# Kernel optimization log

Measured on AMD Instinct MI355X. Metric: run time of the kernel, lower is better.

The kernel has to match this reference:

```python
import jax, jax.numpy as jnp
import numpy as np
import math

N, T, D = 1024, 4096, 20


def setup_inputs() -> dict:
    key = jax.random.key(0)
    k1, k2, k3, k4, k5 = jax.random.split(key, 5)
    evidence_vector = jax.random.normal(k1, (T, D), jnp.float32)
    # valid (strictly positive) prior and row-stochastic, all-positive transitions
    prior_probs = jax.nn.softmax(jax.random.normal(k2, (N,), jnp.float32))
    transition_probs = jax.nn.softmax(jax.random.normal(k3, (N, N), jnp.float32), axis=1)
    means = jax.random.normal(k4, (N, D), jnp.float32)
    stds = jax.random.uniform(k5, (N, D), jnp.float32, minval=0.5, maxval=1.5)
    emission_paras = jnp.stack([means, stds], axis=-1)  # [N, D, 2]
    return {"evidence_vector": evidence_vector, "prior_probs": prior_probs,
            "transition_probs": transition_probs, "emission_paras": emission_paras}


def _emission_logp(evidence, emission_paras):
    # Faithful to the source: p = (2*pi*std)**(-0.5) * exp(-(x-mean)^2/(2*std^2))
    mean = emission_paras[..., 0]  # [N, D]
    std = emission_paras[..., 1]   # [N, D]
    p = (2.0 * math.pi * std) ** (-0.5) * jnp.exp(
        -(evidence[:, None, :] - mean) ** 2 / (2.0 * std ** 2))  # [T, N, D]
    logp = jnp.log(p)
    # step 0 uses raw log; steps >=1 pass through nan_to_num(nan=0, inf kept)
    logp0 = jnp.sum(logp[0], axis=1)  # [N]
    logp_rest = jnp.sum(jnp.nan_to_num(logp[1:], nan=0.0, posinf=jnp.inf, neginf=-jnp.inf), axis=2)  # [T-1, N]
    return logp0, logp_rest


def _viterbi_nl(evidence, prior, trans, emission_paras):
    logp0, logp_rest = _emission_logp(evidence, emission_paras)
    log_trans = jnp.log(trans)  # all positive transitions -> finite
    col0 = jnp.log(prior) + logp0  # [N]

    state_ids = jnp.arange(N)

    def step(prev_col, logp_t):
        # scores[k, j] = nl[k, i-1] + log trans[k, j]; nl[j,i] = max_k scores + logp
        scores = prev_col[:, None] + log_trans          # [N, N]
        best = jnp.max(scores, axis=0)                  # [N]
        # j == 0 branch of the source: prev_state = j, no max over k
        new0 = prev_col[0] + log_trans[0, 0]
        new_col = jnp.where(state_ids == 0, new0, best) + logp_t
        return new_col, new_col

    _, cols = jax.lax.scan(step, col0, logp_rest)       # [T-1, N]
    nl = jnp.concatenate([col0[None, :], cols], axis=0).T  # [N, T]
    return nl, log_trans


def reference(evidence_vector, prior_probs, transition_probs, emission_paras):
    nl, log_trans = _viterbi_nl(evidence_vector, prior_probs, transition_probs, emission_paras)
    last = jnp.argmax(nl[:, -1]).astype(jnp.int32)

    def bt_step(front, i):
        # argmax_j nl[j, i] + log trans[j, front]; strict '>' ascending -> first max
        best = jnp.argmax(nl[:, i] + log_trans[:, front]).astype(jnp.int32)
        return best, best

    _, rev = jax.lax.scan(bt_step, last, jnp.arange(T - 2, -1, -1))
    # source appends the final argmax twice, then prepends states for i = T-2..0
    sequence = jnp.concatenate([rev[::-1], jnp.array([last, last], dtype=jnp.int32)])
    return sequence  # [T + 1] int32
```

## Files before the change

### kernel.cpp

```cpp
#include <hip/hip_runtime.h>
#include <math.h>

#define NSTATES 1024
#define TT      4096
#define DD      20

#define FW_BLOCKS  64
#define FW_THREADS 256
#define JPB  16
#define NSEG 16
#define KSEG 64

#define SENT 0x7FC00000u

#define OFF_COLS  ((size_t)20 << 20)
#define OFF_PTR   ((size_t)36 << 20)

typedef unsigned int u32;

#define ALD(p) __hip_atomic_load((p), __ATOMIC_RELAXED, __HIP_MEMORY_SCOPE_AGENT)

__global__ __launch_bounds__(FW_THREADS, 1) void k_forward(
    const float* __restrict__ tr, const float* __restrict__ ev,
    const float* __restrict__ epar, const float* __restrict__ prior,
    float* __restrict__ cols, unsigned short* __restrict__ bptr,
    u32* __restrict__ ready)
{
    __shared__ __align__(16) float prevs[NSEG * 68];
    __shared__ float          smaxw[4][JPB];
    __shared__ unsigned short sidxw[4][JPB];
    __shared__ float          elp[2][JPB][DD];
    const int tid  = threadIdx.x;
    const int seg  = tid >> 4;
    const int jj   = tid & (JPB - 1);
    const int wav  = tid >> 6;
    const int j0   = blockIdx.x * JPB;
    const int j    = j0 + jj;

    {
        uint4* mine = (uint4*)cols + (size_t)blockIdx.x * (NSTATES * TT / 4 / FW_BLOCKS);
        const uint4 sv = make_uint4(SENT, SENT, SENT, SENT);
        #pragma unroll
        for (int i = 0; i < (NSTATES * TT / 4 / FW_BLOCKS) / FW_THREADS; ++i)
            mine[i * FW_THREADS + tid] = sv;
    }

    const float lat00 = logf(tr[0]);
    float4 latr[16];
    #pragma unroll
    for (int u = 0; u < 16; ++u) {
        #pragma unroll
        for (int i = 0; i < 4; ++i) {
            int k = seg * KSEG + u * 4 + i;
            ((float*)&latr[u])[i] = logf(tr[(size_t)k * NSTATES + j]);
        }
    }

    const int jj0e = tid / DD, d0e = tid % DD;
    const float m0 = epar[((size_t)(j0 + jj0e) * DD + d0e) * 2 + 0];
    const float s0 = epar[((size_t)(j0 + jj0e) * DD + d0e) * 2 + 1];
    const float coef0 = 1.0f / sqrtf(6.2831853071795864769f * s0);
    const float den0  = 2.0f * (s0 * s0);
    const bool  has1  = (tid + 256) < JPB * DD;
    const int   it1   = tid + 256;
    const int jj1e = has1 ? it1 / DD : 0, d1e = has1 ? it1 % DD : 0;
    const float m1 = has1 ? epar[((size_t)(j0 + jj1e) * DD + d1e) * 2 + 0] : 0.0f;
    const float s1 = has1 ? epar[((size_t)(j0 + jj1e) * DD + d1e) * 2 + 1] : 1.0f;
    const float coef1 = 1.0f / sqrtf(6.2831853071795864769f * s1);
    const float den1  = 2.0f * (s1 * s1);

    auto emis = [&](int t, int buf) {
        float x0  = ev[(size_t)t * DD + d0e];
        float df0 = x0 - m0;
        float num0 = df0 * df0;
        float p0  = coef0 * expf(-num0 / den0);
        elp[buf][jj0e][d0e] = logf(p0);
        if (has1) {
            float x1  = ev[(size_t)t * DD + d1e];
            float df1 = x1 - m1;
            float num1 = df1 * df1;
            float p1  = coef1 * expf(-num1 / den1);
            elp[buf][jj1e][d1e] = logf(p1);
        }
    };

    __syncthreads();
    if (tid == 0) {
        asm volatile("s_waitcnt vmcnt(0)" ::: "memory");
        __hip_atomic_fetch_add(ready, 1u, __ATOMIC_RELEASE,
                               __HIP_MEMORY_SCOPE_AGENT);
        while (ALD(ready) < (u32)FW_BLOCKS) __builtin_amdgcn_s_sleep(2);
    }
    __syncthreads();

    float* dstp = &prevs[(tid >> 4) * 68 + (tid & 15) * 4];
    const float* rowp = &prevs[seg * 68];

    emis(0, 0);
    __syncthreads();
    if (tid < JPB) {
        float acc = 0.0f;
        #pragma unroll
        for (int d = 0; d < DD; ++d) acc += elp[0][tid][d];
        float c0 = logf(prior[j0 + tid]) + acc;
        __hip_atomic_store((u32*)cols + (j0 + tid), __float_as_uint(c0),
                           __ATOMIC_RELAXED, __HIP_MEMORY_SCOPE_AGENT);
    }
    __syncthreads();
    emis(1, 1);
    __syncthreads();
    float esum_reg = 0.0f;
    if (tid < JPB) {
        #pragma unroll
        for (int d = 0; d < DD; ++d) esum_reg += elp[1][tid][d];
    }

    for (int t = 1; t < TT; ++t) {
        const u32* p = (const u32*)(cols + (size_t)(t - 1) * NSTATES) + tid * 4;
        u32 w0, w1, w2, w3;
        for (;;) {
            w0 = __hip_atomic_load(p + 0, __ATOMIC_RELAXED, __HIP_MEMORY_SCOPE_AGENT);
            w1 = __hip_atomic_load(p + 1, __ATOMIC_RELAXED, __HIP_MEMORY_SCOPE_AGENT);
            w2 = __hip_atomic_load(p + 2, __ATOMIC_RELAXED, __HIP_MEMORY_SCOPE_AGENT);
            w3 = __hip_atomic_load(p + 3, __ATOMIC_RELAXED, __HIP_MEMORY_SCOPE_AGENT);
            if (w0 != SENT && w1 != SENT && w2 != SENT && w3 != SENT) break;
            __builtin_amdgcn_s_sleep(1);
        }
        {
            float4 v;
            v.x = __uint_as_float(w0);
            v.y = __uint_as_float(w1);
            v.z = __uint_as_float(w2);
            v.w = __uint_as_float(w3);
            *(float4*)dstp = v;
        }
        __syncthreads();

        float best = -__builtin_inff();
        int bidx = seg * KSEG;
        #pragma unroll
        for (int u = 0; u < 16; ++u) {
            float4 q  = *(const float4*)(rowp + u * 4);
            float4 wv = latr[u];
            int k0 = seg * KSEG + u * 4;
            float v0 = q.x + wv.x;
            float v1 = q.y + wv.y;
            float v2 = q.z + wv.z;
            float v3 = q.w + wv.w;
            if (v0 > best) { best = v0; bidx = k0;     }
            if (v1 > best) { best = v1; bidx = k0 + 1; }
            if (v2 > best) { best = v2; bidx = k0 + 2; }
            if (v3 > best) { best = v3; bidx = k0 + 3; }
        }

        {
            float ov = __shfl_xor(best, 16);
            int   oi = __shfl_xor(bidx, 16);
            if (ov > best || (ov == best && oi < bidx)) { best = ov; bidx = oi; }
            ov = __shfl_xor(best, 32);
            oi = __shfl_xor(bidx, 32);
            if (ov > best || (ov == best && oi < bidx)) { best = ov; bidx = oi; }
        }
        if ((tid & 63) < JPB) {
            smaxw[wav][jj] = best;
            sidxw[wav][jj] = (unsigned short)bidx;
        }
        __syncthreads();

        if (tid < JPB) {
            float m = smaxw[0][tid];
            int  mi = sidxw[0][tid];
            #pragma unroll
            for (int ww = 1; ww < 4; ++ww) {
                float v = smaxw[ww][tid];
                if (v > m) { m = v; mi = sidxw[ww][tid]; }
            }
            int jw = j0 + tid;
            float val = (jw == 0) ? (prevs[0] + lat00) : m;
            float out = val + esum_reg;
            __hip_atomic_store((u32*)(cols + (size_t)t * NSTATES) + jw,
                               __float_as_uint(out), __ATOMIC_RELAXED,
                               __HIP_MEMORY_SCOPE_AGENT);
            bptr[(size_t)t * NSTATES + jw] = (unsigned short)mi;
        }

        if (t + 1 < TT) {
            emis(t + 1, (t + 1) & 1);
            __syncthreads();
            if (tid < JPB) {
                float acc = 0.0f;
                #pragma unroll
                for (int d = 0; d < DD; ++d) acc += elp[(t + 1) & 1][tid][d];
                esum_reg = acc;
            }
        }
    }
}

#define BTC 24
__global__ void k_backtrace(const float* __restrict__ lastcol,
                            const unsigned short* __restrict__ bptr,
                            int* __restrict__ seq)
{
    __shared__ unsigned short ring[2][BTC][NSTATES];
    __shared__ int s_front;
    const int tid = threadIdx.x;

    if (tid < 64) {
        float best = -__builtin_inff();
        int bi = 0;
        for (int n2 = tid; n2 < NSTATES; n2 += 64) {
            float v = lastcol[n2];
            if (v > best) { best = v; bi = n2; }
        }
        #pragma unroll
        for (int off = 32; off > 0; off >>= 1) {
            float ov = __shfl_xor(best, off);
            int   oi = __shfl_xor(bi, off);
            if (ov > best || (ov == best && oi < bi)) { best = ov; bi = oi; }
        }
        if (tid == 0) { seq[TT] = bi; seq[TT - 1] = bi; s_front = bi; }
    }
    __syncthreads();

    auto stage = [&](int c, int buf, int t0, int stride) {
        int rhi = TT - 1 - c * BTC;
        int rlo = rhi - (BTC - 1); if (rlo < 1) rlo = 1;
        int n4 = (rhi - rlo + 1) * 128;
        uint4* dst = (uint4*)&ring[buf][0][0];
        for (int idx = t0; idx < n4; idx += stride) {
            int ro = idx >> 7, wo = idx & 127;
            dst[idx] = ((const uint4*)(bptr + (size_t)(rhi - ro) * NSTATES))[wo];
        }
    };
    const int nc = (TT - 1 + BTC - 1) / BTC;
    stage(0, 0, tid, 256);
    __syncthreads();
    for (int c = 0; c < nc; ++c) {
        int buf = c & 1;
        if (tid != 0) {
            if (c + 1 < nc) stage(c + 1, buf ^ 1, tid - 1, 255);
        } else {
            int rhi = TT - 1 - c * BTC;
            int rlo = rhi - (BTC - 1); if (rlo < 1) rlo = 1;
            int front = s_front;
            for (int r = rhi; r >= rlo; --r) {
                front = (int)ring[buf][rhi - r][front];
                seq[r - 1] = front;
            }
            s_front = front;
        }
        __syncthreads();
    }
}

extern "C" void kernel_launch(void* const* d_in, const int* in_sizes, int n_in,
                              void* d_out, int out_size, void* d_ws, size_t ws_size,
                              hipStream_t stream) {
    const float* ev    = (const float*)d_in[0];
    const float* prior = (const float*)d_in[1];
    const float* tr    = (const float*)d_in[2];
    const float* epar  = (const float*)d_in[3];
    int* seq = (int*)d_out;
    char* ws = (char*)d_ws;
    float* cols = (float*)(ws + OFF_COLS);
    unsigned short* bptr = (unsigned short*)(ws + OFF_PTR);
    u32* ready = (u32*)(ws + OFF_PTR);

    hipMemsetAsync(ready, 0, 4, stream);
    k_forward<<<FW_BLOCKS, FW_THREADS, 0, stream>>>(tr, ev, epar, prior,
                                                    cols, bptr, ready);
    k_backtrace<<<1, 256, 0, stream>>>(cols + (size_t)(TT - 1) * NSTATES, bptr, seq);
}
```

Baseline: 9.452 ms.

## Parallelize Viterbi backtrace across 64 blocks via composed segment maps

The backtrace moves from one sequential block to 64 blocks, each owning 64 rows of backpointers in LDS. Each block composes its rows into a full state-to-state map, block 0 chains these maps to find each segment's entry state, and then every block walks its own segment in parallel. This replaces a single serial walk through 4095 dependent rows with parallel map composition, a short 64-step chain and 64-row walks. In exchange it adds an inter-block spin-wait that relies on all 64 blocks being resident at once, and the forward kernel's ready counter moves to the start of the workspace.

Result: faster. 8.678 ms (-8.2%).

```diff
diff --git a/kernel.cpp b/kernel.cpp
--- a/kernel.cpp
+++ b/kernel.cpp
@@ -19,6 +19,7 @@
 typedef unsigned int u32;
 
 #define ALD(p) __hip_atomic_load((p), __ATOMIC_RELAXED, __HIP_MEMORY_SCOPE_AGENT)
+#define AST(p, v) __hip_atomic_store((p), (v), __ATOMIC_RELAXED, __HIP_MEMORY_SCOPE_AGENT)
 
 __global__ __launch_bounds__(FW_THREADS, 1) void k_forward(
     const float* __restrict__ tr, const float* __restrict__ ev,
@@ -103,8 +104,7 @@
         #pragma unroll
         for (int d = 0; d < DD; ++d) acc += elp[0][tid][d];
         float c0 = logf(prior[j0 + tid]) + acc;
-        __hip_atomic_store((u32*)cols + (j0 + tid), __float_as_uint(c0),
-                           __ATOMIC_RELAXED, __HIP_MEMORY_SCOPE_AGENT);
+        AST((u32*)cols + (j0 + tid), __float_as_uint(c0));
     }
     __syncthreads();
     emis(1, 1);
@@ -119,10 +119,10 @@
         const u32* p = (const u32*)(cols + (size_t)(t - 1) * NSTATES) + tid * 4;
         u32 w0, w1, w2, w3;
         for (;;) {
-            w0 = __hip_atomic_load(p + 0, __ATOMIC_RELAXED, __HIP_MEMORY_SCOPE_AGENT);
-            w1 = __hip_atomic_load(p + 1, __ATOMIC_RELAXED, __HIP_MEMORY_SCOPE_AGENT);
-            w2 = __hip_atomic_load(p + 2, __ATOMIC_RELAXED, __HIP_MEMORY_SCOPE_AGENT);
-            w3 = __hip_atomic_load(p + 3, __ATOMIC_RELAXED, __HIP_MEMORY_SCOPE_AGENT);
+            w0 = ALD(p + 0);
+            w1 = ALD(p + 1);
+            w2 = ALD(p + 2);
+            w3 = ALD(p + 3);
             if (w0 != SENT && w1 != SENT && w2 != SENT && w3 != SENT) break;
             __builtin_amdgcn_s_sleep(1);
         }
@@ -178,9 +178,7 @@
             int jw = j0 + tid;
             float val = (jw == 0) ? (prevs[0] + lat00) : m;
             float out = val + esum_reg;
-            __hip_atomic_store((u32*)(cols + (size_t)t * NSTATES) + jw,
-                               __float_as_uint(out), __ATOMIC_RELAXED,
-                               __HIP_MEMORY_SCOPE_AGENT);
+            AST((u32*)(cols + (size_t)t * NSTATES) + jw, __float_as_uint(out));
             bptr[(size_t)t * NSTATES + jw] = (unsigned short)mi;
         }
 
@@ -197,60 +195,79 @@
     }
 }
 
-#define BTC 24
-__global__ void k_backtrace(const float* __restrict__ lastcol,
-                            const unsigned short* __restrict__ bptr,
-                            int* __restrict__ seq)
+#define SEGR 64
+__global__ __launch_bounds__(256, 1) void k_backtrace(
+    const float* __restrict__ lastcol, const unsigned short* __restrict__ bptr,
+    int* __restrict__ seq, u32* __restrict__ ctrl,
+    u32* __restrict__ entries, u32* __restrict__ maps)
 {
-    __shared__ unsigned short ring[2][BTC][NSTATES];
-    __shared__ int s_front;
+    __shared__ unsigned short rows[SEGR][NSTATES];
+    __shared__ int s_last;
     const int tid = threadIdx.x;
-
-    if (tid < 64) {
-        float best = -__builtin_inff();
-        int bi = 0;
-        for (int n2 = tid; n2 < NSTATES; n2 += 64) {
-            float v = lastcol[n2];
-            if (v > best) { best = v; bi = n2; }
-        }
-        #pragma unroll
-        for (int off = 32; off > 0; off >>= 1) {
-            float ov = __shfl_xor(best, off);
-            int   oi = __shfl_xor(bi, off);
-            if (ov > best || (ov == best && oi < bi)) { best = ov; bi = oi; }
-        }
-        if (tid == 0) { seq[TT] = bi; seq[TT - 1] = bi; s_front = bi; }
-    }
-    __syncthreads();
-
-    auto stage = [&](int c, int buf, int t0, int stride) {
-        int rhi = TT - 1 - c * BTC;
-        int rlo = rhi - (BTC - 1); if (rlo < 1) rlo = 1;
-        int n4 = (rhi - rlo + 1) * 128;
-        uint4* dst = (uint4*)&ring[buf][0][0];
-        for (int idx = t0; idx < n4; idx += stride) {
-            int ro = idx >> 7, wo = idx & 127;
-            dst[idx] = ((const uint4*)(bptr + (size_t)(rhi - ro) * NSTATES))[wo];
-        }
-    };
-    const int nc = (TT - 1 + BTC - 1) / BTC;
-    stage(0, 0, tid, 256);
-    __syncthreads();
-    for (int c = 0; c < nc; ++c) {
-        int buf = c & 1;
-        if (tid != 0) {
-            if (c + 1 < nc) stage(c + 1, buf ^ 1, tid - 1, 255);
-        } else {
-            int rhi = TT - 1 - c * BTC;
-            int rlo = rhi - (BTC - 1); if (rlo < 1) rlo = 1;
-            int front = s_front;
-            for (int r = rhi; r >= rlo; --r) {
-                front = (int)ring[buf][rhi - r][front];
-                seq[r - 1] = front;
-            }
-            s_front = front;
+    const int s   = blockIdx.x;
+    const int lo  = (s == 0) ? 1 : s * SEGR;
+    const int hi  = s * SEGR + SEGR - 1;
+    const int nrows = hi - lo + 1;
+
+    for (int idx = tid; idx < nrows * 128; idx += 256) {
+        int ro = idx >> 7, wo = idx & 127;
+        ((uint4*)&rows[ro][0])[wo] =
+            ((const uint4*)(bptr + (size_t)(lo + ro) * NSTATES))[wo];
+    }
+    __syncthreads();
+
+    int f0 = tid * 4, f1 = tid * 4 + 1, f2 = tid * 4 + 2, f3 = tid * 4 + 3;
+    for (int r = hi; r >= lo; --r) {
+        const unsigned short* row = &rows[r - lo][0];
+        f0 = row[f0]; f1 = row[f1]; f2 = row[f2]; f3 = row[f3];
+    }
+    AST(maps + (size_t)s * 512 + 2 * tid,     (u32)f0 | ((u32)f1 << 16));
+    AST(maps + (size_t)s * 512 + 2 * tid + 1, (u32)f2 | ((u32)f3 << 16));
+    __syncthreads();
+    if (tid == 0)
+        __hip_atomic_fetch_add(ctrl + 1, 1u, __ATOMIC_RELEASE,
+                               __HIP_MEMORY_SCOPE_AGENT);
+
+    if (s == 0) {
+        if (tid < 64) {
+            float best = -__builtin_inff();
+            int bi = 0;
+            for (int n2 = tid; n2 < NSTATES; n2 += 64) {
+                float v = lastcol[n2];
+                if (v > best) { best = v; bi = n2; }
+            }
+            #pragma unroll
+            for (int off = 32; off > 0; off >>= 1) {
+                float ov = __shfl_xor(best, off);
+                int   oi = __shfl_xor(bi, off);
+                if (ov > best || (ov == best && oi < bi)) { best = ov; bi = oi; }
+            }
+            if (tid == 0) s_last = bi;
         }
         __syncthreads();
+        if (tid == 0) {
+            while (ALD(ctrl + 1) < 64u) __builtin_amdgcn_s_sleep(2);
+            int last = s_last;
+            seq[TT] = last; seq[TT - 1] = last;
+            u32 entry = (u32)last;
+            for (int ss = 63; ss >= 1; --ss) {
+                AST(entries + ss, entry);
+                u32 w = ALD(maps + (size_t)ss * 512 + (entry >> 1));
+                entry = (entry & 1) ? (w >> 16) : (w & 0xFFFFu);
+            }
+            AST(entries + 0, entry);
+            asm volatile("s_waitcnt vmcnt(0)" ::: "memory");
+            AST(ctrl + 2, 1u);
+        }
+    }
+
+    if (tid == 0) {
+        while (ALD(ctrl + 2) == 0u) __builtin_amdgcn_s_sleep(2);
+        u32 front = ALD(entries + s);
+        for (int r = hi; r >= lo; --r) {
+            front = rows[r - lo][front];
+            seq[r - 1] = (int)front;
+        }
     }
 }
 
@@ -265,10 +282,13 @@
     char* ws = (char*)d_ws;
     float* cols = (float*)(ws + OFF_COLS);
     unsigned short* bptr = (unsigned short*)(ws + OFF_PTR);
-    u32* ready = (u32*)(ws + OFF_PTR);
-
-    hipMemsetAsync(ready, 0, 4, stream);
+    u32* ctrl    = (u32*)ws;
+    u32* entries = (u32*)(ws + 256);
+    u32* maps    = (u32*)(ws + 4096);
+
+    hipMemsetAsync(ctrl, 0, 16, stream);
     k_forward<<<FW_BLOCKS, FW_THREADS, 0, stream>>>(tr, ev, epar, prior,
-                                                    cols, bptr, ready);
-    k_backtrace<<<1, 256, 0, stream>>>(cols + (size_t)(TT - 1) * NSTATES, bptr, seq);
+                                                    cols, bptr, ctrl);
+    k_backtrace<<<64, 256, 0, stream>>>(cols + (size_t)(TT - 1) * NSTATES,
+                                        bptr, seq, ctrl, entries, maps);
 }
```
